# Optimization experiments

Measured on AMD Instinct MI355X. Metric: run time of the kernel, lower is better.

## Reference

```python
import jax, jax.numpy as jnp
import numpy as np

B, C, N, K_NN = 16, 64, 2048, 3
OUT_C = 64


def setup_inputs() -> dict:
    key = jax.random.key(0)
    k1, k2, k3 = jax.random.split(key, 3)
    x = jax.random.normal(k1, (B, C, N), dtype=jnp.float32)
    fan_in = C * K_NN
    bound = 1.0 / np.sqrt(fan_in)
    W = jax.random.uniform(k2, (OUT_C, C, K_NN), minval=-bound, maxval=bound, dtype=jnp.float32)
    b = jax.random.uniform(k3, (OUT_C,), minval=-bound, maxval=bound, dtype=jnp.float32)
    return {"x": x, "W": W, "b": b}


def reference(x, W, b):
    # x: [B, C, N]; W: [O, C, K]; b: [O]
    K = W.shape[-1]
    # Pairwise squared distances: dist[b,i,j] = |x_i|^2 + |x_j|^2 - 2 x_i.x_j.
    # The original takes sqrt, but sqrt is monotone and the distances are only
    # used for top-k index selection, so we select on squared distances (same indices).
    norm_sq = jnp.sum(x * x, axis=1)                      # [B, N]
    dot = jnp.einsum('bcn,bcm->bnm', x, x)                # [B, N, N]
    dist_sq = norm_sq[:, :, None] + norm_sq[:, None, :] - 2.0 * dot  # [B, N, N]
    # K smallest distances per row -> neighbor indices [B, N, K]
    _, idx = jax.lax.top_k(-dist_sq, K)
    # Gather neighbors: neigh[b, c, n, k] = x[b, c, idx[b, n, k]]
    neigh = jax.vmap(lambda xb, ib: xb[:, ib])(x, idx)    # [B, C, N, K]
    # Conv1d with kernel_size == stride == K over the flattened [B, C, N*K]
    # tensor is exactly a per-window contraction over the K neighbors.
    out = jnp.einsum('bcnk,ock->bon', neigh, W) + b[None, :, None]  # [B, O, N]
    return out
```

## Files before the change

### kernel.cpp

```cpp
#include <hip/hip_runtime.h>
#include <cfloat>
#include <climits>

#define B_DIM 16
#define C_DIM 64
#define N_DIM 2048
#define O_DIM 64
#define K_NN  3

typedef __attribute__((ext_vector_type(8))) short bf16x8;
typedef __attribute__((ext_vector_type(4))) float floatx4;

#define GLDS16(gsrc, ldst)                                        \
  __builtin_amdgcn_global_load_lds(                               \
      (const __attribute__((address_space(1))) void*)(gsrc),      \
      (__attribute__((address_space(3))) void*)(ldst), 16, 0, 0)

__device__ __forceinline__ unsigned short f32_to_bf16_rne(float f) {
  unsigned int u = __float_as_uint(f);
  return (unsigned short)((u + 0x7fffu + ((u >> 16) & 1u)) >> 16);
}
__device__ __forceinline__ float bf16_to_f32(unsigned short h) {
  return __uint_as_float(((unsigned int)h) << 16);
}

__device__ __forceinline__ unsigned med3u(unsigned a, unsigned b, unsigned c) {
  unsigned mn = min(a, b), mx = max(a, b);
  return max(mn, min(mx, c));
}

__device__ __forceinline__ void ins4p(unsigned u, int jv, unsigned* k, int* j) {
  bool c3 = u < k[3], c2 = u < k[2], c1 = u < k[1], c0 = u < k[0];
  k[3] = c2 ? k[2] : (c3 ? u  : k[3]);
  j[3] = c2 ? j[2] : (c3 ? jv : j[3]);
  k[2] = c1 ? k[1] : (c2 ? u  : k[2]);
  j[2] = c1 ? j[1] : (c2 ? jv : j[2]);
  k[1] = c0 ? k[0] : (c1 ? u  : k[1]);
  j[1] = c0 ? j[0] : (c1 ? jv : j[1]);
  k[0] = c0 ? u  : k[0];
  j[0] = c0 ? jv : j[0];
}

__device__ __forceinline__ void ins3u64(unsigned long long v,
                                        unsigned long long& k0,
                                        unsigned long long& k1,
                                        unsigned long long& k2) {
  bool c0 = v < k0, c1 = v < k1, c2 = v < k2;
  k2 = c1 ? k1 : (c2 ? v : k2);
  k1 = c0 ? k0 : (c1 ? v : k1);
  k0 = c0 ? v : k0;
}

__global__ __launch_bounds__(256) void prep_kernel(
    const float* __restrict__ x, float* __restrict__ xT,
    unsigned short* __restrict__ xTh, unsigned short* __restrict__ xTl,
    double* __restrict__ nd, float* __restrict__ nf,
    const float* __restrict__ W, float* __restrict__ Wt) {
  int bid = blockIdx.x;
  int t = threadIdx.x;
  if (bid >= 512) {
    int t2 = (bid - 512) * 256 + t;
    int o  = t2 / (C_DIM * K_NN);
    int ck = t2 - o * (C_DIM * K_NN);
    Wt[ck * O_DIM + o] = W[t2];
    return;
  }
  __shared__ __align__(16) float xs[C_DIM][68];
  int b  = bid >> 5;
  int n0 = (bid & 31) * 64;
  const float* xb = x + (size_t)b * C_DIM * N_DIM;
  #pragma unroll
  for (int r = 0; r < 4; ++r) {
    int idx = r * 256 + t;
    int c = idx >> 4;
    int qq = idx & 15;
    *(float4*)&xs[c][qq * 4] = *(const float4*)(xb + (size_t)c * N_DIM + n0 + qq * 4);
  }
  __syncthreads();
  int n = t >> 2, cg = t & 3;
  float v[16];
  #pragma unroll
  for (int cc = 0; cc < 16; ++cc) v[cc] = xs[cg * 16 + cc][n];
  double ps = 0.0;
  #pragma unroll
  for (int cc = 0; cc < 16; ++cc) ps = fma((double)v[cc], (double)v[cc], ps);
  ps += __shfl_xor(ps, 1, 64);
  ps += __shfl_xor(ps, 2, 64);
  size_t row = (size_t)b * N_DIM + n0 + n;
  #pragma unroll
  for (int qq = 0; qq < 4; ++qq) {
    float4 wv; wv.x = v[qq*4]; wv.y = v[qq*4+1]; wv.z = v[qq*4+2]; wv.w = v[qq*4+3];
    *(float4*)&xT[row * C_DIM + cg * 16 + qq * 4] = wv;
  }
  unsigned short hh[16], ll[16];
  #pragma unroll
  for (int cc = 0; cc < 16; ++cc) {
    hh[cc] = f32_to_bf16_rne(v[cc]);
    ll[cc] = f32_to_bf16_rne(v[cc] - bf16_to_f32(hh[cc]));
  }
  #pragma unroll
  for (int e = 0; e < 2; ++e) {
    int phys = (2 * cg + e) ^ (n & 7);
    unsigned int hp[4], lp[4];
    #pragma unroll
    for (int xk = 0; xk < 4; ++xk) {
      hp[xk] = (unsigned)hh[e*8 + 2*xk] | ((unsigned)hh[e*8 + 2*xk + 1] << 16);
      lp[xk] = (unsigned)ll[e*8 + 2*xk] | ((unsigned)ll[e*8 + 2*xk + 1] << 16);
    }
    ((uint4*)xTh)[row * 8 + phys] = *(uint4*)hp;
    ((uint4*)xTl)[row * 8 + phys] = *(uint4*)lp;
  }
  if (cg == 0) {
    nd[row] = ps;
    nf[row] = (float)ps + 512.0f;
  }
}

__global__ __launch_bounds__(256, 4) void topk_kernel(
    const unsigned short* __restrict__ xTh, const unsigned short* __restrict__ xTl,
    const float* __restrict__ nf, unsigned short* __restrict__ cand) {
  __shared__ __align__(16) unsigned short Jh[2][64 * 64];
  __shared__ __align__(16) unsigned short Jl[2][64 * 64];
  int bid   = blockIdx.x;
  int q     = bid & 3;
  int itile = (bid >> 2) & 15;
  int b     = bid >> 6;
  int i0    = itile * 128;
  int jq0   = q * 512;
  int t = threadIdx.x;
  int w = t >> 6, lane = t & 63, quad = lane >> 4, col = lane & 15;
  int csw = col & 7;
  const unsigned short* xh = xTh + (size_t)b * N_DIM * 64;
  const unsigned short* xl = xTl + (size_t)b * N_DIM * 64;
  const float* nfb = nf + b * N_DIM;

  bf16x8 ih[2][2], il[2][2];
  #pragma unroll
  for (int s2 = 0; s2 < 2; ++s2) {
    #pragma unroll
    for (int ks = 0; ks < 2; ++ks) {
      size_t row = i0 + w * 32 + s2 * 16 + col;
      int phys = (ks * 4 + quad) ^ csw;
      ih[s2][ks] = *(const bf16x8*)(xh + row * 64 + phys * 8);
      il[s2][ks] = *(const bf16x8*)(xl + row * 64 + phys * 8);
    }
  }

  unsigned ck[2][4];
  #pragma unroll
  for (int s2 = 0; s2 < 2; ++s2)
    ck[s2][0] = ck[s2][1] = ck[s2][2] = ck[s2][3] = 0xFFFFFFFFu;

  int a0 = col * 64 + ((quad ^ csw) * 8);
  int a1 = col * 64 + (((4 + quad) ^ csw) * 8);

  const unsigned short* sbh = xh + (size_t)(jq0 + w * 16) * 64 + lane * 8;
  const unsigned short* sbl = xl + (size_t)(jq0 + w * 16) * 64 + lane * 8;
  int ldsb = w * 16 * 64;

  #pragma unroll
  for (int k2 = 0; k2 < 2; ++k2) {
    GLDS16(sbh + k2 * 512, &Jh[0][ldsb + k2 * 512]);
    GLDS16(sbl + k2 * 512, &Jl[0][ldsb + k2 * 512]);
  }
  __syncthreads();

  #pragma unroll
  for (int js = 0; js < 8; ++js) {
    int cur = js & 1, nxt = cur ^ 1;
    int j0 = jq0 + js * 64;

    if (js < 7) {
      #pragma unroll
      for (int k2 = 0; k2 < 2; ++k2) {
        GLDS16(sbh + (js + 1) * 4096 + k2 * 512, &Jh[nxt][ldsb + k2 * 512]);
        GLDS16(sbl + (js + 1) * 4096 + k2 * 512, &Jl[nxt][ldsb + k2 * 512]);
      }
    }

    floatx4 acc[2][4];
    #pragma unroll
    for (int s2 = 0; s2 < 2; ++s2)
      #pragma unroll
      for (int jt = 0; jt < 4; ++jt) acc[s2][jt] = (floatx4){0.f, 0.f, 0.f, 0.f};

    #pragma unroll
    for (int ks = 0; ks < 2; ++ks) {
      int ab = ks ? a1 : a0;
      #pragma unroll
      for (int jt = 0; jt < 4; ++jt) {
        bf16x8 jh = *(const bf16x8*)&Jh[cur][jt * 1024 + ab];
        bf16x8 jl = *(const bf16x8*)&Jl[cur][jt * 1024 + ab];
        #pragma unroll
        for (int s2 = 0; s2 < 2; ++s2) {
          acc[s2][jt] = __builtin_amdgcn_mfma_f32_16x16x32_bf16(jl, ih[s2][ks], acc[s2][jt], 0, 0, 0);
          acc[s2][jt] = __builtin_amdgcn_mfma_f32_16x16x32_bf16(jh, il[s2][ks], acc[s2][jt], 0, 0, 0);
          acc[s2][jt] = __builtin_amdgcn_mfma_f32_16x16x32_bf16(jh, ih[s2][ks], acc[s2][jt], 0, 0, 0);
        }
      }
    }

    unsigned locb = (unsigned)(js << 4);
    int jb = j0 + quad * 4;
    #pragma unroll
    for (int jt = 0; jt < 4; ++jt) {
      float4 nv = *(const float4*)(nfb + jb + jt * 16);
      float nfa[4] = {nv.x, nv.y, nv.z, nv.w};
      #pragma unroll
      for (int r = 0; r < 4; ++r) {
        unsigned idbits = locb | (unsigned)(jt * 4 + r);
        #pragma unroll
        for (int s2 = 0; s2 < 2; ++s2) {
          float key = fmaf(-2.0f, acc[s2][jt][r], nfa[r]);
          unsigned u = (__float_as_uint(key) & 0xFFFFFF80u) | idbits;
          unsigned m0 = min(ck[s2][0], u);
          unsigned m1 = med3u(ck[s2][0], u, ck[s2][1]);
          unsigned m2 = med3u(ck[s2][1], u, ck[s2][2]);
          unsigned m3 = med3u(ck[s2][2], u, ck[s2][3]);
          ck[s2][0] = m0; ck[s2][1] = m1; ck[s2][2] = m2; ck[s2][3] = m3;
        }
      }
    }
    __syncthreads();
  }

  #pragma unroll
  for (int s2 = 0; s2 < 2; ++s2) {
    int cj[4];
    unsigned cku[4];
    #pragma unroll
    for (int s = 0; s < 4; ++s) {
      unsigned loc = ck[s2][s] & 127u;
      cj[s] = jq0 + (int)((loc >> 4) << 6) + (int)(((loc >> 2) & 3u) << 4) +
              (quad << 2) + (int)(loc & 3u);
      cku[s] = ck[s2][s];
    }
    #pragma unroll
    for (int m = 16; m < 64; m <<= 1) {
      unsigned tu[4]; int tj[4];
      #pragma unroll
      for (int s = 0; s < 4; ++s) {
        tu[s] = __shfl_xor(cku[s], m, 64);
        tj[s] = __shfl_xor(cj[s], m, 64);
      }
      #pragma unroll
      for (int s = 0; s < 4; ++s) ins4p(tu[s], tj[s], cku, cj);
    }
    if (quad == 0) {
      int row = b * N_DIM + i0 + w * 32 + s2 * 16 + col;
      unsigned short* cp = cand + row * 16 + q * 4;
      cp[0] = (unsigned short)cj[0];
      cp[1] = (unsigned short)cj[1];
      cp[2] = (unsigned short)cj[2];
      cp[3] = (unsigned short)cj[3];
    }
  }
}

#define NT   64
#define NPAD 68
__global__ __launch_bounds__(256, 2) void conv_kernel(
    const float* __restrict__ xT, const double* __restrict__ nd,
    const unsigned short* __restrict__ cand,
    const float* __restrict__ Wt, const float* __restrict__ bias,
    float* __restrict__ out) {
  __shared__ __align__(16) float nb[C_DIM * K_NN][NPAD];
  __shared__ unsigned long long tks[NT];
  int bid = blockIdx.x;
  int b  = bid >> 5;
  int n0 = (bid & 31) * NT;
  const float* xtb = xT + (size_t)b * N_DIM * C_DIM;
  const double* ndb = nd + b * N_DIM;
  int t = threadIdx.x;
  int w = t >> 6, lane = t & 63;
  int cid = lane >> 2, seg = lane & 3;

  for (int g = 0; g < 8; ++g) {
    int nnA = w * 16 + 2 * g;
    int nnB = nnA + 1;
    int jA = cand[(b * N_DIM + n0 + nnA) * 16 + cid];
    int jB = cand[(b * N_DIM + n0 + nnB) * 16 + cid];
    const float* xnA = xtb + (size_t)(n0 + nnA) * C_DIM + seg * 16;
    const float* xjA = xtb + (size_t)jA * C_DIM + seg * 16;
    const float* xnB = xtb + (size_t)(n0 + nnB) * C_DIM + seg * 16;
    const float* xjB = xtb + (size_t)jB * C_DIM + seg * 16;
    float4 aA[4], bA[4], aB[4], bB[4];
    #pragma unroll
    for (int qq = 0; qq < 4; ++qq) {
      aA[qq] = *(const float4*)(xnA + qq * 4);
      bA[qq] = *(const float4*)(xjA + qq * 4);
      aB[qq] = *(const float4*)(xnB + qq * 4);
      bB[qq] = *(const float4*)(xjB + qq * 4);
    }
    double pA = 0.0, pB = 0.0;
    #pragma unroll
    for (int qq = 0; qq < 4; ++qq) {
      pA = fma((double)aA[qq].x, (double)bA[qq].x, pA);
      pA = fma((double)aA[qq].y, (double)bA[qq].y, pA);
      pA = fma((double)aA[qq].z, (double)bA[qq].z, pA);
      pA = fma((double)aA[qq].w, (double)bA[qq].w, pA);
      pB = fma((double)aB[qq].x, (double)bB[qq].x, pB);
      pB = fma((double)aB[qq].y, (double)bB[qq].y, pB);
      pB = fma((double)aB[qq].z, (double)bB[qq].z, pB);
      pB = fma((double)aB[qq].w, (double)bB[qq].w, pB);
    }
    pA += __shfl_xor(pA, 1, 64);
    pA += __shfl_xor(pA, 2, 64);
    pB += __shfl_xor(pB, 1, 64);
    pB += __shfl_xor(pB, 2, 64);
    double keyA = fma(-2.0, pA, ndb[jA] + 512.0);
    double keyB = fma(-2.0, pB, ndb[jB] + 512.0);
    unsigned long long uA =
        ((unsigned long long)__double_as_longlong(keyA) & ~2047ull) |
        (unsigned long long)(unsigned)jA;
    unsigned long long uB =
        ((unsigned long long)__double_as_longlong(keyB) & ~2047ull) |
        (unsigned long long)(unsigned)jB;
    unsigned long long a0 = uA, a1 = ~0ull, a2 = ~0ull;
    unsigned long long b0 = uB, b1 = ~0ull, b2 = ~0ull;
    #pragma unroll
    for (int m = 4; m < 64; m <<= 1) {
      unsigned long long q0 = __shfl_xor(a0, m, 64);
      unsigned long long q1 = __shfl_xor(a1, m, 64);
      unsigned long long q2 = __shfl_xor(a2, m, 64);
      ins3u64(q0, a0, a1, a2); ins3u64(q1, a0, a1, a2); ins3u64(q2, a0, a1, a2);
      unsigned long long r0 = __shfl_xor(b0, m, 64);
      unsigned long long r1 = __shfl_xor(b1, m, 64);
      unsigned long long r2 = __shfl_xor(b2, m, 64);
      ins3u64(r0, b0, b1, b2); ins3u64(r1, b0, b1, b2); ins3u64(r2, b0, b1, b2);
    }
    if (lane == 0) {
      tks[nnA] = (a0 & 2047ull) | ((a1 & 2047ull) << 16) | ((a2 & 2047ull) << 32);
      tks[nnB] = (b0 & 2047ull) | ((b1 & 2047ull) << 16) | ((b2 & 2047ull) << 32);
    }
  }
  __syncthreads();

  #pragma unroll
  for (int p = 0; p < 12; ++p) {
    int u = p * 256 + t;
    int sg = u & 15;
    int r  = u >> 4;
    int k = r >> 6, n = r & 63;
    int j = (int)((tks[n] >> (16 * k)) & 2047ull);
    float4 v = *(const float4*)(xtb + (size_t)j * C_DIM + sg * 4);
    nb[(sg * 4 + 0) * 3 + k][n] = v.x;
    nb[(sg * 4 + 1) * 3 + k][n] = v.y;
    nb[(sg * 4 + 2) * 3 + k][n] = v.z;
    nb[(sg * 4 + 3) * 3 + k][n] = v.w;
  }
  __syncthreads();

  int ng = t & 15, og = t >> 4;
  float acc[4][4];
  #pragma unroll
  for (int oo = 0; oo < 4; ++oo) {
    float bv = bias[(og << 2) + oo];
    #pragma unroll
    for (int nn2 = 0; nn2 < 4; ++nn2) acc[oo][nn2] = bv;
  }
  const float* nbp = &nb[0][0] + (ng << 2);
  const float* wtp = Wt + (og << 2);
  #pragma unroll 4
  for (int ckk = 0; ckk < C_DIM * K_NN; ++ckk) {
    float4 nv = *(const float4*)(nbp + ckk * NPAD);
    float4 wv = *(const float4*)(wtp + ckk * O_DIM);
    float na[4] = {nv.x, nv.y, nv.z, nv.w};
    float wa[4] = {wv.x, wv.y, wv.z, wv.w};
    #pragma unroll
    for (int oo = 0; oo < 4; ++oo)
      #pragma unroll
      for (int nn2 = 0; nn2 < 4; ++nn2)
        acc[oo][nn2] = fmaf(wa[oo], na[nn2], acc[oo][nn2]);
  }
  #pragma unroll
  for (int oo = 0; oo < 4; ++oo) {
    int o = (og << 2) + oo;
    float4 v; v.x = acc[oo][0]; v.y = acc[oo][1]; v.z = acc[oo][2]; v.w = acc[oo][3];
    *(float4*)&out[(size_t)(b * O_DIM + o) * N_DIM + n0 + (ng << 2)] = v;
  }
}

extern "C" void kernel_launch(void* const* d_in, const int* in_sizes, int n_in,
                              void* d_out, int out_size, void* d_ws, size_t ws_size,
                              hipStream_t stream) {
  const float* x    = (const float*)d_in[0];
  const float* W    = (const float*)d_in[1];
  const float* bias = (const float*)d_in[2];
  float* out = (float*)d_out;
  char* ws = (char*)d_ws;
  float*          xT  = (float*)ws;
  unsigned short* xTh = (unsigned short*)(ws + 8388608);
  unsigned short* xTl = (unsigned short*)(ws + 12582912);
  double*         nd  = (double*)(ws + 16777216);
  float*          nfp = (float*)(ws + 17039360);
  unsigned short* cd  = (unsigned short*)(ws + 17170432);
  float*          Wt  = (float*)(ws + 18219008);

  prep_kernel<<<512 + 48, 256, 0, stream>>>(x, xT, xTh, xTl, nd, nfp, W, Wt);
  topk_kernel<<<B_DIM * 16 * 4, 256, 0, stream>>>(xTh, xTl, nfp, cd);
  conv_kernel<<<B_DIM * (N_DIM / NT), 256, 0, stream>>>(xT, nd, cd, Wt, bias, out);
}
```

Measured before the change: 139.7 us.

## Triple-buffer top-k J tiles with 32-row stages and a single barrier per stage

Restructures the top-k kernel's LDS pipeline from double-buffered 64-row tiles to triple-buffered 32-row tiles, keeping two loads in flight. Each stage now waits with explicit vmcnt counts and uses one raw s_barrier instead of two __syncthreads. The goal is to hide global-to-LDS load latency and cut barrier cost. In exchange there are more iterations with less MFMA work each, and the candidate index encoding is changed to match the new tile shape.

After: 212.7 us. 1.52x slower.

```diff
diff --git a/kernel.cpp b/kernel.cpp
--- a/kernel.cpp
+++ b/kernel.cpp
@@ -119,8 +119,8 @@
 __global__ __launch_bounds__(256, 4) void topk_kernel(
     const unsigned short* __restrict__ xTh, const unsigned short* __restrict__ xTl,
     const float* __restrict__ nf, unsigned short* __restrict__ cand) {
-  __shared__ __align__(16) unsigned short Jh[2][64 * 64];
-  __shared__ __align__(16) unsigned short Jl[2][64 * 64];
+  __shared__ __align__(16) unsigned short Jh[3][32 * 64];
+  __shared__ __align__(16) unsigned short Jl[3][32 * 64];
   int bid   = blockIdx.x;
   int q     = bid & 3;
   int itile = (bid >> 2) & 15;
@@ -154,41 +154,40 @@
   int a0 = col * 64 + ((quad ^ csw) * 8);
   int a1 = col * 64 + (((4 + quad) ^ csw) * 8);
 
-  const unsigned short* sbh = xh + (size_t)(jq0 + w * 16) * 64 + lane * 8;
-  const unsigned short* sbl = xl + (size_t)(jq0 + w * 16) * 64 + lane * 8;
-  int ldsb = w * 16 * 64;
-
-  #pragma unroll
-  for (int k2 = 0; k2 < 2; ++k2) {
-    GLDS16(sbh + k2 * 512, &Jh[0][ldsb + k2 * 512]);
-    GLDS16(sbl + k2 * 512, &Jl[0][ldsb + k2 * 512]);
-  }
-  __syncthreads();
-
-  #pragma unroll
-  for (int js = 0; js < 8; ++js) {
-    int cur = js & 1, nxt = cur ^ 1;
-    int j0 = jq0 + js * 64;
-
-    if (js < 7) {
-      #pragma unroll
-      for (int k2 = 0; k2 < 2; ++k2) {
-        GLDS16(sbh + (js + 1) * 4096 + k2 * 512, &Jh[nxt][ldsb + k2 * 512]);
-        GLDS16(sbl + (js + 1) * 4096 + k2 * 512, &Jl[nxt][ldsb + k2 * 512]);
-      }
-    }
-
-    floatx4 acc[2][4];
+  const unsigned short* sbh = xh + (size_t)(jq0 + w * 8) * 64 + lane * 8;
+  const unsigned short* sbl = xl + (size_t)(jq0 + w * 8) * 64 + lane * 8;
+  int ldsb = w * 8 * 64;
+
+  GLDS16(sbh,        &Jh[0][ldsb]);
+  GLDS16(sbl,        &Jl[0][ldsb]);
+  GLDS16(sbh + 2048, &Jh[1][ldsb]);
+  GLDS16(sbl + 2048, &Jl[1][ldsb]);
+
+  #pragma unroll
+  for (int st = 0; st < 16; ++st) {
+    if (st < 15) asm volatile("s_waitcnt vmcnt(2)" ::: "memory");
+    else         asm volatile("s_waitcnt vmcnt(0)" ::: "memory");
+    __builtin_amdgcn_s_barrier();
+    __builtin_amdgcn_sched_barrier(0);
+
+    const int cur = st % 3;
+    if (st < 14) {
+      const int nb = (st + 2) % 3;
+      GLDS16(sbh + (st + 2) * 2048, &Jh[nb][ldsb]);
+      GLDS16(sbl + (st + 2) * 2048, &Jl[nb][ldsb]);
+    }
+
+    floatx4 acc[2][2];
     #pragma unroll
     for (int s2 = 0; s2 < 2; ++s2)
       #pragma unroll
-      for (int jt = 0; jt < 4; ++jt) acc[s2][jt] = (floatx4){0.f, 0.f, 0.f, 0.f};
+      for (int jt = 0; jt < 2; ++jt) acc[s2][jt] = (floatx4){0.f, 0.f, 0.f, 0.f};
 
     #pragma unroll
     for (int ks = 0; ks < 2; ++ks) {
       int ab = ks ? a1 : a0;
       #pragma unroll
-      for (int jt = 0; jt < 4; ++jt) {
+      for (int jt = 0; jt < 2; ++jt) {
         bf16x8 jh = *(const bf16x8*)&Jh[cur][jt * 1024 + ab];
         bf16x8 jl = *(const bf16x8*)&Jl[cur][jt * 1024 + ab];
         #pragma unroll
@@ -200,10 +199,10 @@
       }
     }
 
-    unsigned locb = (unsigned)(js << 4);
-    int jb = j0 + quad * 4;
-    #pragma unroll
-    for (int jt = 0; jt < 4; ++jt) {
+    unsigned locb = (unsigned)(st << 3);
+    int jb = jq0 + st * 32 + quad * 4;
+    #pragma unroll
+    for (int jt = 0; jt < 2; ++jt) {
       float4 nv = *(const float4*)(nfb + jb + jt * 16);
       float nfa[4] = {nv.x, nv.y, nv.z, nv.w};
       #pragma unroll
@@ -221,7 +220,6 @@
         }
       }
     }
-    __syncthreads();
   }
 
   #pragma unroll
@@ -231,7 +229,7 @@
     #pragma unroll
     for (int s = 0; s < 4; ++s) {
       unsigned loc = ck[s2][s] & 127u;
-      cj[s] = jq0 + (int)((loc >> 4) << 6) + (int)(((loc >> 2) & 3u) << 4) +
+      cj[s] = jq0 + (int)((loc >> 3) << 5) + (int)(((loc >> 2) & 1u) << 4) +
               (quad << 2) + (int)(loc & 3u);
       cku[s] = ck[s2][s];
     }
```
